# Kernel tuning notes

Hardware: AMD Instinct MI355X
Metric: run time of the kernel (lower is better)

The kernel has to match this reference:

```python
import jax, jax.numpy as jnp
import numpy as np

N_NODES = 100000
N_EDGES = 3200000
N_FEAT = 128
HIDDEN = 16
N_CLASSES = 10
N_GRAPHS = 64


def gcn_conv(x, W, b, src, dst, num_nodes):
    # PyG GCNConv: h = x W; add self-loops; norm = deg^{-1/2}[src]*deg^{-1/2}[dst]
    h = x @ W  # [N, out]
    deg = jax.ops.segment_sum(jnp.ones(src.shape[0], h.dtype), dst,
                              num_segments=num_nodes) + 1.0  # self-loop
    dinv = jax.lax.rsqrt(deg)
    coef = dinv[src] * dinv[dst]  # [E]
    agg = jax.ops.segment_sum(h[src] * coef[:, None], dst,
                              num_segments=num_nodes)
    # self-loop contribution: norm = dinv[i]^2
    agg = agg + h * (dinv * dinv)[:, None]
    return agg + b


def setup_inputs() -> dict:
    key = jax.random.key(0)
    k1, k2, k3, k4, k5, k6, k7 = jax.random.split(key, 7)
    x = jax.random.normal(k1, (N_NODES, N_FEAT), dtype=jnp.float32)
    edge_index = jax.random.randint(k2, (2, N_EDGES), 0, N_NODES, dtype=jnp.int64)
    batch = jnp.sort(jax.random.randint(k3, (N_NODES,), 0, N_GRAPHS, dtype=jnp.int64))
    W1 = jax.random.normal(k4, (N_FEAT, HIDDEN), dtype=jnp.float32) / np.sqrt(N_FEAT)
    b1 = jnp.zeros((HIDDEN,), jnp.float32)
    W2 = jax.random.normal(k5, (HIDDEN, N_CLASSES), dtype=jnp.float32) / np.sqrt(HIDDEN)
    b2 = jnp.zeros((N_CLASSES,), jnp.float32)
    return {"x": x, "edge_index": edge_index, "batch": batch,
            "W1": W1, "b1": b1, "W2": W2, "b2": b2}


def reference(x, edge_index, batch, W1, b1, W2, b2):
    src, dst = edge_index[0], edge_index[1]
    h = gcn_conv(x, W1, b1, src, dst, N_NODES)
    h = jax.nn.relu(h)
    h = gcn_conv(h, W2, b2, src, dst, N_NODES)  # [N, C]
    # global mean pool per graph
    sums = jax.ops.segment_sum(h, batch, num_segments=N_GRAPHS)
    cnts = jax.ops.segment_sum(jnp.ones(N_NODES, h.dtype), batch,
                               num_segments=N_GRAPHS)
    pooled = sums / jnp.maximum(cnts, 1.0)[:, None]  # [G, C]
    return jax.nn.log_softmax(pooled, axis=1)
```

## Files before the change

### kernel.cpp

```cpp
#include <hip/hip_runtime.h>

#define N_NODES   100000
#define N_EDGES   3200000
#define N_FEAT    128
#define HIDDEN    16
#define N_CLASSES 10
#define N_GRAPHS  64

#define NBUCK     391
#define CAP       9216
#define BINA_EPB  8192
#define BINA_BLOCKS ((N_EDGES + BINA_EPB - 1) / BINA_EPB)


__global__ __launch_bounds__(512) void k_ginit(int* __restrict__ gcur,
                                               float* __restrict__ pooled) {
    int t = threadIdx.x;
    if (t < NBUCK) gcur[t] = t * CAP;
    pooled[t] = 0.f;
    pooled[t + 512] = 0.f;
}

__global__ __launch_bounds__(512) void k_binA(const int* __restrict__ src,
                                              const int* __restrict__ dst,
                                              int* __restrict__ gcur,
                                              int* __restrict__ stage) {
    __shared__ int hist[NBUCK];
    __shared__ int curb[NBUCK];
    int tid = threadIdx.x;
    long long base = (long long)blockIdx.x * BINA_EPB;
    for (int t = tid; t < NBUCK; t += 512) hist[t] = 0;
    __syncthreads();
    int se[16], de[16];
#pragma unroll
    for (int i = 0; i < 16; ++i) {
        long long e = base + i * 512 + tid;
        if (e < N_EDGES) {
            se[i] = src[e];
            de[i] = dst[e];
            atomicAdd(&hist[de[i] >> 8], 1);
        } else {
            de[i] = -1;
        }
    }
    __syncthreads();
    for (int t = tid; t < NBUCK; t += 512) {
        int h = hist[t];
        curb[t] = h ? atomicAdd(&gcur[t], h) : 0;
    }
    __syncthreads();
#pragma unroll
    for (int i = 0; i < 16; ++i) {
        if (de[i] >= 0) {
            int b = de[i] >> 8;
            int p = atomicAdd(&curb[b], 1);
            stage[p] = (se[i] << 8) | (de[i] & 255);
        }
    }
}

__global__ __launch_bounds__(512) void k_bscan(const int* __restrict__ gcur,
                                               int* __restrict__ bbase,
                                               int* __restrict__ off) {
    __shared__ int s[512];
    int t = threadIdx.x;
    int c = (t < NBUCK) ? (gcur[t] - t * CAP) : 0;
    s[t] = c;
    __syncthreads();
    for (int o = 1; o < 512; o <<= 1) {
        int a = (t >= o) ? s[t - o] : 0;
        __syncthreads();
        s[t] += a;
        __syncthreads();
    }
    if (t < NBUCK) bbase[t] = s[t] - c;
    if (t == 0) off[N_NODES] = N_EDGES;
}

__global__ __launch_bounds__(256) void k_binB(const int* __restrict__ gcur,
                                              const int* __restrict__ bbase,
                                              const int* __restrict__ stage,
                                              int* __restrict__ off,
                                              float* __restrict__ dinv,
                                              int* __restrict__ srcs) {
    __shared__ int hist[256];
    __shared__ int excl[256];
    int b = blockIdx.x, t = threadIdx.x;
    int cnt   = gcur[b] - b * CAP;
    int sbase = b * CAP;
    int cbase = bbase[b];
    hist[t] = 0;
    __syncthreads();
    for (int i = t; i < cnt; i += 256) {
        int v = stage[sbase + i];
        atomicAdd(&hist[v & 255], 1);
    }
    __syncthreads();
    int c = hist[t];
    excl[t] = c;
    __syncthreads();
    for (int o = 1; o < 256; o <<= 1) {
        int a = (t >= o) ? excl[t - o] : 0;
        __syncthreads();
        excl[t] += a;
        __syncthreads();
    }
    int ex = excl[t] - c;
    int node = b * 256 + t;
    if (node < N_NODES) {
        off[node]  = cbase + ex;
        dinv[node] = rsqrtf((float)c + 1.0f);
    }
    __syncthreads();
    hist[t] = ex;
    __syncthreads();
    for (int i = t; i < cnt; i += 256) {
        int v = stage[sbase + i];
        int p = cbase + atomicAdd(&hist[v & 255], 1);
        srcs[p] = v >> 8;
    }
}

__global__ __launch_bounds__(256) void k_gemm1(const float* __restrict__ x,
                                               const float* __restrict__ W1,
                                               const float* __restrict__ dinv,
                                               float* __restrict__ h1p) {
    __shared__ float w[N_FEAT * HIDDEN];
    __shared__ float xs[16 * N_FEAT];
    __shared__ float ds[16];
    int tid  = threadIdx.x;
    int base = blockIdx.x * 16;
    if (tid < 16) ds[tid] = dinv[base + tid];
    const float4* w4 = (const float4*)W1;
    float4*       wd = (float4*)w;
    wd[tid]       = w4[tid];
    wd[256 + tid] = w4[256 + tid];
    const float4* x4 = (const float4*)(x + (long long)base * N_FEAT);
    float4*       xd = (float4*)xs;
    xd[tid]       = x4[tid];
    xd[256 + tid] = x4[256 + tid];
    __syncthreads();
    int n = tid >> 4, c = tid & 15;
    const float* xr = &xs[n * N_FEAT];
    float acc = 0.f;
#pragma unroll
    for (int k = 0; k < N_FEAT; ++k) acc += xr[k] * w[k * HIDDEN + c];
    h1p[(base + n) * HIDDEN + c] = acc * ds[n];
}

__global__ __launch_bounds__(256) void k_agg1(const int* __restrict__ off,
                                              const int* __restrict__ srcs,
                                              const float* __restrict__ dinv,
                                              const float* __restrict__ h1p,
                                              const float* __restrict__ b1,
                                              const float* __restrict__ W2,
                                              float* __restrict__ h2p) {
    __shared__ float r_s[16][17];
    __shared__ float w2s[HIDDEN * N_CLASSES];
    int tid = threadIdx.x;
    if (tid < HIDDEN * N_CLASSES) w2s[tid] = W2[tid];
    int nl = tid >> 4, c = tid & 15;
    int n  = blockIdx.x * 16 + nl;
    int beg = off[n], end = off[n + 1];
    float a0 = h1p[n * 16 + c];
    float a1 = 0.f, a2 = 0.f, a3 = 0.f;
    int j = beg;
    for (; j + 3 < end; j += 4) {
        int s0 = srcs[j], s1 = srcs[j + 1], s2 = srcs[j + 2], s3 = srcs[j + 3];
        a0 += h1p[s0 * 16 + c];
        a1 += h1p[s1 * 16 + c];
        a2 += h1p[s2 * 16 + c];
        a3 += h1p[s3 * 16 + c];
    }
    for (; j < end; ++j) a0 += h1p[srcs[j] * 16 + c];
    float acc = (a0 + a1) + (a2 + a3);
    float dn  = dinv[n];
    r_s[nl][c] = fmaxf(dn * acc + b1[c], 0.f);
    __syncthreads();
    if (c < N_CLASSES) {
        float o = 0.f;
#pragma unroll
        for (int k = 0; k < HIDDEN; ++k) o += r_s[nl][k] * w2s[k * N_CLASSES + c];
        h2p[n * 16 + c] = dn * o;
    } else {
        h2p[n * 16 + c] = 0.f;
    }
}

__global__ __launch_bounds__(256) void k_agg2p(const int* __restrict__ off,
                                               const int* __restrict__ srcs,
                                               const float* __restrict__ dinv,
                                               const float* __restrict__ h2p,
                                               const int* __restrict__ batch,
                                               float* __restrict__ pooled) {
    __shared__ float red[16][17];
    int tid = threadIdx.x;
    int nl = tid >> 4, c = tid & 15;
    int nbase = blockIdx.x * 16;
    int n  = nbase + nl;
    int beg = off[n], end = off[n + 1];
    float a0 = h2p[n * 16 + c];
    float a1 = 0.f, a2 = 0.f, a3 = 0.f;
    int j = beg;
    for (; j + 3 < end; j += 4) {
        int s0 = srcs[j], s1 = srcs[j + 1], s2 = srcs[j + 2], s3 = srcs[j + 3];
        a0 += h2p[s0 * 16 + c];
        a1 += h2p[s1 * 16 + c];
        a2 += h2p[s2 * 16 + c];
        a3 += h2p[s3 * 16 + c];
    }
    for (; j < end; ++j) a0 += h2p[srcs[j] * 16 + c];
    float o = dinv[n] * ((a0 + a1) + (a2 + a3));

    int g0  = batch[nbase];
    int g15 = batch[nbase + 15];
    if (g0 == g15) {
        red[nl][c] = o;
        __syncthreads();
#pragma unroll
        for (int s = 8; s > 0; s >>= 1) {
            if (nl < s) red[nl][c] += red[nl + s][c];
            __syncthreads();
        }
        if (tid < N_CLASSES) atomicAdd(&pooled[g0 * 16 + tid], red[0][tid]);
    } else {
        if (c < N_CLASSES) atomicAdd(&pooled[batch[n] * 16 + c], o);
    }
}

__global__ __launch_bounds__(64) void k_final(const float* __restrict__ pooled,
                                              const float* __restrict__ b2,
                                              const int* __restrict__ batch,
                                              float* __restrict__ out) {
    int g = threadIdx.x;
    if (g >= N_GRAPHS) return;
    int lo = 0, hi = N_NODES;
    while (lo < hi) { int m = (lo + hi) >> 1; if (batch[m] < g) lo = m + 1; else hi = m; }
    int start = lo;
    lo = 0; hi = N_NODES;
    while (lo < hi) { int m = (lo + hi) >> 1; if (batch[m] < g + 1) lo = m + 1; else hi = m; }
    int cnt = lo - start;

    float v[N_CLASSES];
    if (cnt > 0) {
        float inv = 1.f / (float)cnt;
#pragma unroll
        for (int j = 0; j < N_CLASSES; ++j) v[j] = pooled[g * 16 + j] * inv + b2[j];
    } else {
#pragma unroll
        for (int j = 0; j < N_CLASSES; ++j) v[j] = 0.f;
    }
    float m = v[0];
#pragma unroll
    for (int j = 1; j < N_CLASSES; ++j) m = fmaxf(m, v[j]);
    float l = 0.f;
#pragma unroll
    for (int j = 0; j < N_CLASSES; ++j) l += expf(v[j] - m);
    l = logf(l);
#pragma unroll
    for (int j = 0; j < N_CLASSES; ++j) out[g * N_CLASSES + j] = v[j] - m - l;
}

extern "C" void kernel_launch(void* const* d_in, const int* in_sizes, int n_in,
                              void* d_out, int out_size, void* d_ws, size_t ws_size,
                              hipStream_t stream) {
    const float* x     = (const float*)d_in[0];
    const int*   edge  = (const int*)d_in[1];
    const int*   batch = (const int*)d_in[2];
    const float* W1    = (const float*)d_in[3];
    const float* b1    = (const float*)d_in[4];
    const float* W2    = (const float*)d_in[5];
    const float* b2    = (const float*)d_in[6];
    float* out = (float*)d_out;
    float* ws  = (float*)d_ws;

    int*   gcur   = (int*)ws;
    int*   bbase  = (int*)(ws + 512);
    float* pooled = ws + 1024;
    float* dinv   = ws + 2048;
    int*   off    = (int*)(ws + 102048);
    int*   srcs   = (int*)(ws + 202080);
    int*   stage  = (int*)(ws + 3402080);
    float* h1p    = ws + 3402080;
    float* h2p    = ws + 5002080;

    const int* srcp = edge;
    const int* dstp = edge + N_EDGES;

    k_ginit<<<1, 512, 0, stream>>>(gcur, pooled);
    k_binA<<<BINA_BLOCKS, 512, 0, stream>>>(srcp, dstp, gcur, stage);
    k_bscan<<<1, 512, 0, stream>>>(gcur, bbase, off);
    k_binB<<<NBUCK, 256, 0, stream>>>(gcur, bbase, stage, off, dinv, srcs);
    k_gemm1<<<N_NODES / 16, 256, 0, stream>>>(x, W1, dinv, h1p);
    k_agg1<<<N_NODES / 16, 256, 0, stream>>>(off, srcs, dinv, h1p, b1, W2, h2p);
    k_agg2p<<<N_NODES / 16, 256, 0, stream>>>(off, srcs, dinv, h2p, batch, pooled);
    k_final<<<1, 64, 0, stream>>>(pooled, b2, batch, out);
}
```

Baseline: 282.1 us.

## Store hidden features in fp16, prefetch edge indices, widen binning blocks

Intermediate node features h1 and h2 are now stored as half precision, halving the bytes fetched by the random gathers in both aggregation kernels. The aggregation loops are unrolled to eight accumulators, software-prefetch the next eight source indices, and use nontemporal loads for the index stream. The binning kernel moves to 1024-thread blocks covering twice as many edges each. Storing features in fp16 adds rounding error, and the larger binning blocks may reduce occupancy.

```diff
diff --git a/kernel.cpp b/kernel.cpp
--- a/kernel.cpp
+++ b/kernel.cpp
@@ -1,4 +1,5 @@
 #include <hip/hip_runtime.h>
+#include <hip/hip_fp16.h>
 
 #define N_NODES   100000
 #define N_EDGES   3200000
@@ -9,7 +10,7 @@
 
 #define NBUCK     391
 #define CAP       9216
-#define BINA_EPB  8192
+#define BINA_EPB  16384
 #define BINA_BLOCKS ((N_EDGES + BINA_EPB - 1) / BINA_EPB)
 
 
@@ -21,20 +22,20 @@
     pooled[t + 512] = 0.f;
 }
 
-__global__ __launch_bounds__(512) void k_binA(const int* __restrict__ src,
-                                              const int* __restrict__ dst,
-                                              int* __restrict__ gcur,
-                                              int* __restrict__ stage) {
+__global__ __launch_bounds__(1024) void k_binA(const int* __restrict__ src,
+                                               const int* __restrict__ dst,
+                                               int* __restrict__ gcur,
+                                               int* __restrict__ stage) {
     __shared__ int hist[NBUCK];
     __shared__ int curb[NBUCK];
     int tid = threadIdx.x;
     long long base = (long long)blockIdx.x * BINA_EPB;
-    for (int t = tid; t < NBUCK; t += 512) hist[t] = 0;
+    for (int t = tid; t < NBUCK; t += 1024) hist[t] = 0;
     __syncthreads();
     int se[16], de[16];
 #pragma unroll
     for (int i = 0; i < 16; ++i) {
-        long long e = base + i * 512 + tid;
+        long long e = base + i * 1024 + tid;
         if (e < N_EDGES) {
             se[i] = src[e];
             de[i] = dst[e];
@@ -44,7 +45,7 @@
         }
     }
     __syncthreads();
-    for (int t = tid; t < NBUCK; t += 512) {
+    for (int t = tid; t < NBUCK; t += 1024) {
         int h = hist[t];
         curb[t] = h ? atomicAdd(&gcur[t], h) : 0;
     }
@@ -124,7 +125,7 @@
 __global__ __launch_bounds__(256) void k_gemm1(const float* __restrict__ x,
                                                const float* __restrict__ W1,
                                                const float* __restrict__ dinv,
-                                               float* __restrict__ h1p) {
+                                               __half* __restrict__ h1h) {
     __shared__ float w[N_FEAT * HIDDEN];
     __shared__ float xs[16 * N_FEAT];
     __shared__ float ds[16];
@@ -145,16 +146,18 @@
     float acc = 0.f;
 #pragma unroll
     for (int k = 0; k < N_FEAT; ++k) acc += xr[k] * w[k * HIDDEN + c];
-    h1p[(base + n) * HIDDEN + c] = acc * ds[n];
-}
+    h1h[(base + n) * HIDDEN + c] = __float2half(acc * ds[n]);
+}
+
+#define NT(p) __builtin_nontemporal_load(p)
 
 __global__ __launch_bounds__(256) void k_agg1(const int* __restrict__ off,
                                               const int* __restrict__ srcs,
                                               const float* __restrict__ dinv,
-                                              const float* __restrict__ h1p,
+                                              const __half* __restrict__ h1h,
                                               const float* __restrict__ b1,
                                               const float* __restrict__ W2,
-                                              float* __restrict__ h2p) {
+                                              __half* __restrict__ h2h) {
     __shared__ float r_s[16][17];
     __shared__ float w2s[HIDDEN * N_CLASSES];
     int tid = threadIdx.x;
@@ -162,35 +165,61 @@
     int nl = tid >> 4, c = tid & 15;
     int n  = blockIdx.x * 16 + nl;
     int beg = off[n], end = off[n + 1];
-    float a0 = h1p[n * 16 + c];
+    float a0 = __half2float(h1h[n * 16 + c]);
     float a1 = 0.f, a2 = 0.f, a3 = 0.f;
+    float a4 = 0.f, a5 = 0.f, a6 = 0.f, a7 = 0.f;
     int j = beg;
-    for (; j + 3 < end; j += 4) {
-        int s0 = srcs[j], s1 = srcs[j + 1], s2 = srcs[j + 2], s3 = srcs[j + 3];
-        a0 += h1p[s0 * 16 + c];
-        a1 += h1p[s1 * 16 + c];
-        a2 += h1p[s2 * 16 + c];
-        a3 += h1p[s3 * 16 + c];
-    }
-    for (; j < end; ++j) a0 += h1p[srcs[j] * 16 + c];
-    float acc = (a0 + a1) + (a2 + a3);
+    int nfull = (end - beg) >> 3;
+    if (nfull > 0) {
+        int s0 = NT(&srcs[j]),     s1 = NT(&srcs[j + 1]);
+        int s2 = NT(&srcs[j + 2]), s3 = NT(&srcs[j + 3]);
+        int s4 = NT(&srcs[j + 4]), s5 = NT(&srcs[j + 5]);
+        int s6 = NT(&srcs[j + 6]), s7 = NT(&srcs[j + 7]);
+        for (int it = 1; it < nfull; ++it) {
+            int t0 = NT(&srcs[j + 8]),  t1 = NT(&srcs[j + 9]);
+            int t2 = NT(&srcs[j + 10]), t3 = NT(&srcs[j + 11]);
+            int t4 = NT(&srcs[j + 12]), t5 = NT(&srcs[j + 13]);
+            int t6 = NT(&srcs[j + 14]), t7 = NT(&srcs[j + 15]);
+            a0 += __half2float(h1h[s0 * 16 + c]);
+            a1 += __half2float(h1h[s1 * 16 + c]);
+            a2 += __half2float(h1h[s2 * 16 + c]);
+            a3 += __half2float(h1h[s3 * 16 + c]);
+            a4 += __half2float(h1h[s4 * 16 + c]);
+            a5 += __half2float(h1h[s5 * 16 + c]);
+            a6 += __half2float(h1h[s6 * 16 + c]);
+            a7 += __half2float(h1h[s7 * 16 + c]);
+            s0 = t0; s1 = t1; s2 = t2; s3 = t3;
+            s4 = t4; s5 = t5; s6 = t6; s7 = t7;
+            j += 8;
+        }
+        a0 += __half2float(h1h[s0 * 16 + c]);
+        a1 += __half2float(h1h[s1 * 16 + c]);
+        a2 += __half2float(h1h[s2 * 16 + c]);
+        a3 += __half2float(h1h[s3 * 16 + c]);
+        a4 += __half2float(h1h[s4 * 16 + c]);
+        a5 += __half2float(h1h[s5 * 16 + c]);
+        a6 += __half2float(h1h[s6 * 16 + c]);
+        a7 += __half2float(h1h[s7 * 16 + c]);
+        j += 8;
+    }
+    for (; j < end; ++j) a0 += __half2float(h1h[NT(&srcs[j]) * 16 + c]);
+    float acc = (((a0 + a1) + (a2 + a3)) + ((a4 + a5) + (a6 + a7)));
     float dn  = dinv[n];
     r_s[nl][c] = fmaxf(dn * acc + b1[c], 0.f);
     __syncthreads();
+    float o = 0.f;
     if (c < N_CLASSES) {
-        float o = 0.f;
 #pragma unroll
         for (int k = 0; k < HIDDEN; ++k) o += r_s[nl][k] * w2s[k * N_CLASSES + c];
-        h2p[n * 16 + c] = dn * o;
-    } else {
-        h2p[n * 16 + c] = 0.f;
-    }
+        o *= dn;
+    }
+    h2h[n * 16 + c] = __float2half(o);
 }
 
 __global__ __launch_bounds__(256) void k_agg2p(const int* __restrict__ off,
                                                const int* __restrict__ srcs,
                                                const float* __restrict__ dinv,
-                                               const float* __restrict__ h2p,
+                                               const __half* __restrict__ h2h,
                                                const int* __restrict__ batch,
                                                float* __restrict__ pooled) {
     __shared__ float red[16][17];
@@ -199,18 +228,45 @@
     int nbase = blockIdx.x * 16;
     int n  = nbase + nl;
     int beg = off[n], end = off[n + 1];
-    float a0 = h2p[n * 16 + c];
+    float a0 = __half2float(h2h[n * 16 + c]);
     float a1 = 0.f, a2 = 0.f, a3 = 0.f;
+    float a4 = 0.f, a5 = 0.f, a6 = 0.f, a7 = 0.f;
     int j = beg;
-    for (; j + 3 < end; j += 4) {
-        int s0 = srcs[j], s1 = srcs[j + 1], s2 = srcs[j + 2], s3 = srcs[j + 3];
-        a0 += h2p[s0 * 16 + c];
-        a1 += h2p[s1 * 16 + c];
-        a2 += h2p[s2 * 16 + c];
-        a3 += h2p[s3 * 16 + c];
-    }
-    for (; j < end; ++j) a0 += h2p[srcs[j] * 16 + c];
-    float o = dinv[n] * ((a0 + a1) + (a2 + a3));
+    int nfull = (end - beg) >> 3;
+    if (nfull > 0) {
+        int s0 = NT(&srcs[j]),     s1 = NT(&srcs[j + 1]);
+        int s2 = NT(&srcs[j + 2]), s3 = NT(&srcs[j + 3]);
+        int s4 = NT(&srcs[j + 4]), s5 = NT(&srcs[j + 5]);
+        int s6 = NT(&srcs[j + 6]), s7 = NT(&srcs[j + 7]);
+        for (int it = 1; it < nfull; ++it) {
+            int t0 = NT(&srcs[j + 8]),  t1 = NT(&srcs[j + 9]);
+            int t2 = NT(&srcs[j + 10]), t3 = NT(&srcs[j + 11]);
+            int t4 = NT(&srcs[j + 12]), t5 = NT(&srcs[j + 13]);
+            int t6 = NT(&srcs[j + 14]), t7 = NT(&srcs[j + 15]);
+            a0 += __half2float(h2h[s0 * 16 + c]);
+            a1 += __half2float(h2h[s1 * 16 + c]);
+            a2 += __half2float(h2h[s2 * 16 + c]);
+            a3 += __half2float(h2h[s3 * 16 + c]);
+            a4 += __half2float(h2h[s4 * 16 + c]);
+            a5 += __half2float(h2h[s5 * 16 + c]);
+            a6 += __half2float(h2h[s6 * 16 + c]);
+            a7 += __half2float(h2h[s7 * 16 + c]);
+            s0 = t0; s1 = t1; s2 = t2; s3 = t3;
+            s4 = t4; s5 = t5; s6 = t6; s7 = t7;
+            j += 8;
+        }
+        a0 += __half2float(h2h[s0 * 16 + c]);
+        a1 += __half2float(h2h[s1 * 16 + c]);
+        a2 += __half2float(h2h[s2 * 16 + c]);
+        a3 += __half2float(h2h[s3 * 16 + c]);
+        a4 += __half2float(h2h[s4 * 16 + c]);
+        a5 += __half2float(h2h[s5 * 16 + c]);
+        a6 += __half2float(h2h[s6 * 16 + c]);
+        a7 += __half2float(h2h[s7 * 16 + c]);
+        j += 8;
+    }
+    for (; j < end; ++j) a0 += __half2float(h2h[NT(&srcs[j]) * 16 + c]);
+    float o = dinv[n] * ((((a0 + a1) + (a2 + a3)) + ((a4 + a5) + (a6 + a7))));
 
     int g0  = batch[nbase];
     int g15 = batch[nbase + 15];
@@ -274,25 +330,25 @@
     float* out = (float*)d_out;
     float* ws  = (float*)d_ws;
 
-    int*   gcur   = (int*)ws;
-    int*   bbase  = (int*)(ws + 512);
-    float* pooled = ws + 1024;
-    float* dinv   = ws + 2048;
-    int*   off    = (int*)(ws + 102048);
-    int*   srcs   = (int*)(ws + 202080);
-    int*   stage  = (int*)(ws + 3402080);
-    float* h1p    = ws + 3402080;
-    float* h2p    = ws + 5002080;
+    int*    gcur   = (int*)ws;
+    int*    bbase  = (int*)(ws + 512);
+    float*  pooled = ws + 1024;
+    float*  dinv   = ws + 2048;
+    int*    off    = (int*)(ws + 102048);
+    int*    srcs   = (int*)(ws + 202080);
+    int*    stage  = (int*)(ws + 3402080);
+    __half* h1h    = (__half*)(ws + 3402080);
+    __half* h2h    = (__half*)(ws + 4202080);
 
     const int* srcp = edge;
     const int* dstp = edge + N_EDGES;
 
     k_ginit<<<1, 512, 0, stream>>>(gcur, pooled);
-    k_binA<<<BINA_BLOCKS, 512, 0, stream>>>(srcp, dstp, gcur, stage);
+    k_binA<<<BINA_BLOCKS, 1024, 0, stream>>>(srcp, dstp, gcur, stage);
     k_bscan<<<1, 512, 0, stream>>>(gcur, bbase, off);
     k_binB<<<NBUCK, 256, 0, stream>>>(gcur, bbase, stage, off, dinv, srcs);
-    k_gemm1<<<N_NODES / 16, 256, 0, stream>>>(x, W1, dinv, h1p);
-    k_agg1<<<N_NODES / 16, 256, 0, stream>>>(off, srcs, dinv, h1p, b1, W2, h2p);
-    k_agg2p<<<N_NODES / 16, 256, 0, stream>>>(off, srcs, dinv, h2p, batch, pooled);
+    k_gemm1<<<N_NODES / 16, 256, 0, stream>>>(x, W1, dinv, h1h);
+    k_agg1<<<N_NODES / 16, 256, 0, stream>>>(off, srcs, dinv, h1h, b1, W2, h2h);
+    k_agg2p<<<N_NODES / 16, 256, 0, stream>>>(off, srcs, dinv, h2h, batch, pooled);
     k_final<<<1, 64, 0, stream>>>(pooled, b2, batch, out);
 }
```

New measurement: 269.6 us. 1.05x faster.
